# Performance work log

Measured on AMD Instinct MI355X. Metric: run time of the kernel, lower is better.

The kernel has to match this reference:

```python
import jax, jax.numpy as jnp
import numpy as np

# Dims: B nodes, Z species (elements), IN/OUT channels, M = 2*l+1 (l=1)
B, Z, IN, OUT, M = 8192, 10, 512, 512, 3
ALPHA = 1.0 / np.sqrt(IN)  # self.alpha = 1/sqrt(in_dim)
SQRT3 = float(np.sqrt(3.0))


def setup_inputs() -> dict:
    key = jax.random.key(0)
    k1, k2, k3 = jax.random.split(key, 3)
    t = jax.random.normal(k1, (B, IN, M), dtype=jnp.float32)
    species = jax.random.randint(k2, (B,), 0, Z)
    node_attrs = jax.nn.one_hot(species, Z, dtype=jnp.float32)  # [B, Z] one-hot
    # torch.nn.init.uniform_(weights, -sqrt(3), sqrt(3))
    weights = jax.random.uniform(k3, (Z, OUT, IN), dtype=jnp.float32,
                                 minval=-SQRT3, maxval=SQRT3)
    return {"t": t, "node_attrs": node_attrs, "weights": weights}


def reference(t, node_attrs, weights):
    # Faithful to: einsum('bz, zCc, bcd -> bCd', node_attrs, weights*alpha, t)
    # Contract weights with t first per species ([Z,B,C,M], ~500MB), which
    # avoids the huge [B,C,c] per-node weight-gather intermediate, then
    # select/sum over species with the one-hot node_attrs.
    W = weights * ALPHA                       # [Z, OUT, IN]
    zt = jnp.einsum('zCc,bcd->zbCd', W, t)    # [Z, B, OUT, M]
    out = jnp.einsum('bz,zbCd->bCd', node_attrs, zt)  # [B, OUT, M]
    return out
```

## Files before the change

kernel.cpp:

```cpp
#include <hip/hip_runtime.h>
#include <stdint.h>

#define NB   8192
#define NZ   10
#define CIN  512
#define COUT 512
#define MM   3
#define ALPHA 0.04419417382415922f

#define ROWS_TOTAL (NB * MM)
#define BM 256
#define BN 256
#define BK 32
#define NKT (CIN / BK)
#define MAX_MT (ROWS_TOTAL / BM + NZ)
#define NYB (COUT / BN)
#define NWG (MAX_MT * NYB)
#define NGRP 32

typedef short bf16x8 __attribute__((ext_vector_type(8)));
typedef float f32x4  __attribute__((ext_vector_type(4)));

__device__ __forceinline__ uint16_t f2bf(float f) {
    union { float f; uint32_t i; } v; v.f = f;
    uint32_t x = v.i;
    x += 0x7fffu + ((x >> 16) & 1u);
    return (uint16_t)(x >> 16);
}
__device__ __forceinline__ uint32_t pack2(float a, float b) {
    return (uint32_t)f2bf(a) | ((uint32_t)f2bf(b) << 16);
}
__device__ __forceinline__ void async16(const void* g, void* l) {
    __builtin_amdgcn_global_load_lds((const uint32_t*)g, (uint32_t*)l, 16, 0, 0);
}

__global__ __launch_bounds__(256)
void prep_kernel(const float* __restrict__ attrs, const float* __restrict__ w,
                 int* __restrict__ species, int* __restrict__ hist,
                 ushort* __restrict__ wt) {
    const int tid = threadIdx.x;
    if (blockIdx.x >= NGRP) {
        const size_t base = (size_t)(blockIdx.x - NGRP) * 2048;
        const float* src = w + base;
        ushort* dst = wt + base;
        float4 a = *(const float4*)(src + tid * 4);
        float4 b = *(const float4*)(src + 1024 + tid * 4);
        uint2 oa, ob;
        oa.x = pack2(a.x, a.y); oa.y = pack2(a.z, a.w);
        ob.x = pack2(b.x, b.y); ob.y = pack2(b.z, b.w);
        *(uint2*)(dst + tid * 4) = oa;
        *(uint2*)(dst + 1024 + tid * 4) = ob;
        return;
    }
    __shared__ int wc[4][NZ];
    const int b = blockIdx.x * 256 + tid;
    const float* a = attrs + (size_t)b * NZ;
    int s = 0;
    #pragma unroll
    for (int z = 0; z < NZ; z++) if (a[z] > 0.5f) s = z;
    species[b] = s;
    const int wv = tid >> 6, lane = tid & 63;
    #pragma unroll
    for (int z = 0; z < NZ; z++) {
        unsigned long long m = __ballot(s == z);
        if (lane == 0) wc[wv][z] = __popcll(m);
    }
    __syncthreads();
    if (tid < NZ) {
        hist[blockIdx.x * NZ + tid] = wc[0][tid] + wc[1][tid] + wc[2][tid] + wc[3][tid];
    }
}

__global__ __launch_bounds__(256)
void place_kernel(const int* __restrict__ species, const int* __restrict__ hist,
                  int* __restrict__ sorted, int* __restrict__ offsets,
                  int* __restrict__ tile_offsets) {
    __shared__ int lhist[NGRP][NZ];
    __shared__ int loff[NZ + 1], ltoff[NZ + 1];
    __shared__ int pb[NZ];
    __shared__ int wc[4][NZ];
    const int tid = threadIdx.x, g = blockIdx.x;

    for (int i = tid; i < NGRP * NZ; i += 256) ((int*)lhist)[i] = hist[i];
    __syncthreads();
    if (tid == 0) {
        int off = 0, toff = 0;
        for (int z = 0; z < NZ; z++) {
            int tot = 0;
            for (int gg = 0; gg < NGRP; gg++) tot += lhist[gg][z];
            loff[z] = off; ltoff[z] = toff;
            off += tot;
            toff += (3 * tot + BM - 1) / BM;
        }
        loff[NZ] = off; ltoff[NZ] = toff;
    }
    __syncthreads();
    if (tid < NZ) {
        int base = loff[tid];
        for (int gg = 0; gg < g; gg++) base += lhist[gg][tid];
        pb[tid] = base;
    }
    if (g == 0 && tid < NZ + 1) {
        offsets[tid] = loff[tid];
        tile_offsets[tid] = ltoff[tid];
    }
    const int b = g * 256 + tid;
    const int s = species[b];
    const int wv = tid >> 6, lane = tid & 63;
    unsigned long long mymask = 0;
    #pragma unroll
    for (int z = 0; z < NZ; z++) {
        unsigned long long m = __ballot(s == z);
        if (lane == 0) wc[wv][z] = __popcll(m);
        if (s == z) mymask = m;
    }
    __syncthreads();
    int rank = __popcll(mymask & ((1ull << lane) - 1ull));
    #pragma unroll
    for (int w2 = 0; w2 < 4; w2++) if (w2 < wv) rank += wc[w2][s];
    sorted[pb[s] + rank] = b;
}

__global__ __launch_bounds__(256)
void pack_t(const float* __restrict__ t, const int* __restrict__ sorted,
            ushort* __restrict__ tt) {
    const int w = threadIdx.x >> 6, L = threadIdx.x & 63;
    const int p = blockIdx.x * 4 + w;
    const int node = sorted[p];
    const float4* src = (const float4*)(t + (size_t)node * (CIN * MM) + L * 24);
    float4 f[6];
    #pragma unroll
    for (int i = 0; i < 6; i++) f[i] = src[i];
    const float* v = (const float*)f;
    #pragma unroll
    for (int d = 0; d < MM; d++) {
        uint4 o;
        o.x = pack2(v[d],      v[3 + d]);
        o.y = pack2(v[6 + d],  v[9 + d]);
        o.z = pack2(v[12 + d], v[15 + d]);
        o.w = pack2(v[18 + d], v[21 + d]);
        *(uint4*)&tt[(size_t)(3 * p + d) * CIN + L * 8] = o;
    }
}

__global__ __launch_bounds__(512, 2)
void gemm_kernel(const ushort* __restrict__ tt, const ushort* __restrict__ wt,
                 const int* __restrict__ sorted, const int* __restrict__ offsets,
                 const int* __restrict__ tile_offsets, float* __restrict__ out) {
    extern __shared__ __align__(16) ushort smem[];
    __shared__ int spos[96];

    const int bid = blockIdx.x;
    const int xcd = bid & 7, ii = bid >> 3;
    const int wg = (xcd < 4 ? xcd * 27 : 108 + (xcd - 4) * 26) + ii;
    const int tz = wg >> 1;
    const int Cbase = (wg & 1) * BN;

    if (tz >= tile_offsets[NZ]) return;
    int z = 0;
    #pragma unroll
    for (int i = 1; i < NZ; i++) if (tile_offsets[i] <= tz) z = i;

    const int row_base = 3 * offsets[z] + (tz - tile_offsets[z]) * BM;
    const int row_end  = 3 * offsets[z + 1];
    const int pos0     = row_base / 3;

    const int tid = threadIdx.x;
    const int w = tid >> 6, L = tid & 63;
    if (tid < 96) spos[tid] = sorted[min(pos0 + tid, NB - 1)];

    const int lr16 = w * 16 + (L >> 2);
    const int cs   = (L & 3) ^ ((L >> 3) & 3);
    const size_t aoff = (size_t)(row_base + lr16) * CIN + cs * 8;
    const size_t boff = ((size_t)z * COUT + Cbase + lr16) * CIN + cs * 8;

#define ASLOT(s) (smem + (s) * 16384)
#define BSLOT(s) (smem + (s) * 16384 + 8192)
#define STAGE_A(s, kt) do {                                                  \
        async16(tt + aoff + (kt) * BK,                    ASLOT(s) + w * 512);          \
        async16(tt + aoff + (size_t)128 * CIN + (kt) * BK, ASLOT(s) + 4096 + w * 512);  \
    } while (0)
#define STAGE_B(s, kt) do {                                                  \
        async16(wt + boff + (kt) * BK,                    BSLOT(s) + w * 512);          \
        async16(wt + boff + (size_t)128 * CIN + (kt) * BK, BSLOT(s) + 4096 + w * 512);  \
    } while (0)

    const int wm = w & 1, wn = w >> 1;
    const int q = L >> 4, mr = L & 15;
    const int qs = (q ^ ((mr >> 1) & 3)) * 8;

    f32x4 acc[8][4];
    #pragma unroll
    for (int i = 0; i < 8; i++)
        #pragma unroll
        for (int j = 0; j < 4; j++) acc[i][j] = (f32x4){0.f, 0.f, 0.f, 0.f};

    STAGE_A(0, 0); STAGE_B(0, 0);
    STAGE_A(1, 1); STAGE_B(1, 1);

    int cur = 0, stg = 2;
    for (int kt = 0; kt < NKT; kt++) {
        if (kt + 1 < NKT) {
            asm volatile("s_waitcnt vmcnt(4)" ::: "memory");
        } else {
            asm volatile("s_waitcnt vmcnt(0)" ::: "memory");
        }
        asm volatile("s_barrier" ::: "memory");
        if (kt + 2 < NKT) STAGE_A(stg, kt + 2);

        const ushort* Ab = ASLOT(cur);
        const ushort* Bb = BSLOT(cur);
        bf16x8 af[4], bf[4];
        #pragma unroll
        for (int am = 0; am < 4; am++)
            af[am] = *(const bf16x8*)(Ab + (wm * 128 + am * 16 + mr) * 32 + qs);
        #pragma unroll
        for (int bn = 0; bn < 4; bn++)
            bf[bn] = *(const bf16x8*)(Bb + (wn * 64 + bn * 16 + mr) * 32 + qs);
        __builtin_amdgcn_s_setprio(1);
        #pragma unroll
        for (int am = 0; am < 4; am++)
            #pragma unroll
            for (int bn = 0; bn < 4; bn++)
                acc[am][bn] = __builtin_amdgcn_mfma_f32_16x16x32_bf16(
                    af[am], bf[bn], acc[am][bn], 0, 0, 0);
        __builtin_amdgcn_s_setprio(0);

        asm volatile("s_barrier" ::: "memory");
        if (kt + 2 < NKT) STAGE_B(stg, kt + 2);

        bf16x8 ag[4];
        #pragma unroll
        for (int am = 0; am < 4; am++)
            ag[am] = *(const bf16x8*)(Ab + (wm * 128 + (am + 4) * 16 + mr) * 32 + qs);
        __builtin_amdgcn_s_setprio(1);
        #pragma unroll
        for (int am = 0; am < 4; am++)
            #pragma unroll
            for (int bn = 0; bn < 4; bn++)
                acc[am + 4][bn] = __builtin_amdgcn_mfma_f32_16x16x32_bf16(
                    ag[am], bf[bn], acc[am + 4][bn], 0, 0, 0);
        __builtin_amdgcn_s_setprio(0);

        cur = (cur == 2) ? 0 : cur + 1;
        stg = (stg == 2) ? 0 : stg + 1;
    }
#undef STAGE_A
#undef STAGE_B

    float* ebuf = (float*)smem;
    #pragma unroll
    for (int ch = 0; ch < 6; ch++) {
        __syncthreads();
        const int pbase = pos0 + ch * 16;
        #pragma unroll
        for (int am = 0; am < 8; am++) {
            #pragma unroll
            for (int r = 0; r < 4; r++) {
                const int Rg = row_base + wm * 128 + am * 16 + q * 4 + r;
                const int pos = Rg / 3;
                const int d = Rg - 3 * pos;
                const int lp = pos - pbase;
                if (lp >= 0 && lp < 16 && Rg < row_end) {
                    #pragma unroll
                    for (int bn = 0; bn < 4; bn++) {
                        const int c = wn * 64 + bn * 16 + mr;
                        ebuf[(lp * BN + c) * 3 + d] = ALPHA * acc[am][bn][r];
                    }
                }
            }
        }
        __syncthreads();
        #pragma unroll 4
        for (int j = 0; j < 24; j++) {
            const int idx = j * 512 + tid;
            const int lp  = idx / 768;
            const int o   = idx - lp * 768;
            const int pos = pbase + lp;
            const int d   = o % 3;
            const int row = 3 * pos + d;
            if (row >= row_base && row < row_base + BM && row < row_end) {
                const int node = spos[pos - pos0];
                out[(size_t)node * (COUT * MM) + Cbase * 3 + o] = ebuf[idx];
            }
        }
    }
}

extern "C" void kernel_launch(void* const* d_in, const int* in_sizes, int n_in,
                              void* d_out, int out_size, void* d_ws, size_t ws_size,
                              hipStream_t stream) {
    const float* t     = (const float*)d_in[0];
    const float* attrs = (const float*)d_in[1];
    const float* w     = (const float*)d_in[2];
    float* out = (float*)d_out;

    uint8_t* ws = (uint8_t*)d_ws;
    int* species      = (int*)ws;                  ws += NB * 4;
    int* sorted       = (int*)ws;                  ws += NB * 4;
    int* hist         = (int*)ws;                  ws += NGRP * NZ * 4;
    int* offsets      = (int*)ws;                  ws += 16 * 4;
    int* tile_offsets = (int*)ws;                  ws += 16 * 4;
    ws = (uint8_t*)(((uintptr_t)ws + 255) & ~(uintptr_t)255);
    ushort* wt = (ushort*)ws;                      ws += (size_t)NZ * COUT * CIN * 2;
    ushort* tt = (ushort*)ws;

    hipLaunchKernelGGL(prep_kernel, dim3(NGRP + (NZ * COUT * CIN) / 2048), dim3(256),
                       0, stream, attrs, w, species, hist, wt);
    hipLaunchKernelGGL(place_kernel, dim3(NGRP), dim3(256), 0, stream,
                       species, hist, sorted, offsets, tile_offsets);
    hipLaunchKernelGGL(pack_t, dim3(NB / 4), dim3(256), 0, stream, t, sorted, tt);
    hipLaunchKernelGGL(gemm_kernel, dim3(NWG), dim3(512), 3 * 2 * 256 * BK * 2, stream,
                       tt, wt, sorted, offsets, tile_offsets, out);
}
```

Measured before the change: 149.9 us.

## Fuse prep, placement, packing and GEMM into one cooperative grid-synced kernel

```diff
diff --git a/kernel.cpp b/kernel.cpp
--- a/kernel.cpp
+++ b/kernel.cpp
@@ -1,4 +1,5 @@
 #include <hip/hip_runtime.h>
+#include <hip/hip_cooperative_groups.h>
 #include <stdint.h>
 
 #define NB   8192
@@ -17,6 +18,7 @@
 #define NYB (COUT / BN)
 #define NWG (MAX_MT * NYB)
 #define NGRP 32
+#define DYN_LDS (3 * 2 * 256 * BK * 2)
 
 typedef short bf16x8 __attribute__((ext_vector_type(8)));
 typedef float f32x4  __attribute__((ext_vector_type(4)));
@@ -32,6 +34,213 @@
 }
 __device__ __forceinline__ void async16(const void* g, void* l) {
     __builtin_amdgcn_global_load_lds((const uint32_t*)g, (uint32_t*)l, 16, 0, 0);
+}
+
+__global__ __launch_bounds__(512, 2)
+void fused_kernel(const float* __restrict__ t, const float* __restrict__ attrs,
+                  const float* __restrict__ w, float* __restrict__ out,
+                  int* __restrict__ sorted, int* __restrict__ meta,
+                  ushort* __restrict__ wt, ushort* __restrict__ ttn) {
+    extern __shared__ __align__(16) ushort smem[];
+    __shared__ int spos[96];
+    __shared__ int loff[NZ + 1], ltoff[NZ + 1];
+
+    cooperative_groups::grid_group grid = cooperative_groups::this_grid();
+    const int bid = blockIdx.x, tid = threadIdx.x;
+    const int gtid = bid * 512 + tid;
+    const int w8 = tid >> 6, L = tid & 63;
+
+    int mys = 0;
+    if (gtid < NB) {
+        const float* a = attrs + (size_t)gtid * NZ;
+        #pragma unroll
+        for (int z = 0; z < NZ; z++) if (a[z] > 0.5f) mys = z;
+        atomicAdd(&meta[mys], 1);
+    }
+    for (int i = gtid; i < NZ * COUT * CIN / 8; i += NWG * 512) {
+        const float4* src = (const float4*)(w + (size_t)i * 8);
+        float4 a = src[0], b = src[1];
+        uint4 o;
+        o.x = pack2(a.x, a.y); o.y = pack2(a.z, a.w);
+        o.z = pack2(b.x, b.y); o.w = pack2(b.z, b.w);
+        *(uint4*)(wt + (size_t)i * 8) = o;
+    }
+    for (int node = bid * 8 + w8; node < NB; node += NWG * 8) {
+        const float4* src = (const float4*)(t + (size_t)node * (CIN * MM) + L * 24);
+        float4 f[6];
+        #pragma unroll
+        for (int i = 0; i < 6; i++) f[i] = src[i];
+        const float* v = (const float*)f;
+        #pragma unroll
+        for (int d = 0; d < MM; d++) {
+            uint4 o;
+            o.x = pack2(v[d],      v[3 + d]);
+            o.y = pack2(v[6 + d],  v[9 + d]);
+            o.z = pack2(v[12 + d], v[15 + d]);
+            o.w = pack2(v[18 + d], v[21 + d]);
+            *(uint4*)&ttn[(size_t)(3 * node + d) * CIN + L * 8] = o;
+        }
+    }
+
+    grid.sync();
+
+    if (tid == 0) {
+        int off = 0, toff = 0;
+        for (int z = 0; z < NZ; z++) {
+            const int c = atomicAdd(&meta[z], 0);
+            loff[z] = off; ltoff[z] = toff;
+            off += c;
+            toff += (3 * c + BM - 1) / BM;
+        }
+        loff[NZ] = off; ltoff[NZ] = toff;
+    }
+    __syncthreads();
+    if (gtid < NB) {
+        const int p = loff[mys] + atomicAdd(&meta[16 + mys], 1);
+        sorted[p] = gtid;
+    }
+
+    grid.sync();
+
+    const int xcd = bid & 7, ii = bid >> 3;
+    const int wg = (xcd < 4 ? xcd * 27 : 108 + (xcd - 4) * 26) + ii;
+    const int tz = wg >> 1;
+    const int Cbase = (wg & 1) * BN;
+
+    if (tz >= ltoff[NZ]) return;
+    int z = 0;
+    #pragma unroll
+    for (int i = 1; i < NZ; i++) if (ltoff[i] <= tz) z = i;
+
+    const int row_base = 3 * loff[z] + (tz - ltoff[z]) * BM;
+    const int row_end  = 3 * loff[z + 1];
+    const int pos0     = row_base / 3;
+
+    if (tid < 96) spos[tid] = sorted[min(pos0 + tid, NB - 1)];
+
+    const int lr16 = w8 * 16 + (L >> 2);
+    const int cs   = (L & 3) ^ ((L >> 3) & 3);
+    const int R0 = row_base + lr16, R1 = R0 + 128;
+    const int pA0 = R0 / 3, dA0 = R0 - 3 * pA0;
+    const int pA1 = R1 / 3, dA1 = R1 - 3 * pA1;
+    const int nA0 = sorted[min(pA0, NB - 1)];
+    const int nA1 = sorted[min(pA1, NB - 1)];
+    const ushort* gA0 = ttn + (size_t)(3 * nA0 + dA0) * CIN + cs * 8;
+    const ushort* gA1 = ttn + (size_t)(3 * nA1 + dA1) * CIN + cs * 8;
+    const size_t boff = ((size_t)z * COUT + Cbase + lr16) * CIN + cs * 8;
+
+#define ASLOT(s) (smem + (s) * 16384)
+#define BSLOT(s) (smem + (s) * 16384 + 8192)
+#define FSTAGE_A(s, kt) do {                                                  \
+        async16(gA0 + (kt) * BK, ASLOT(s) + w8 * 512);                        \
+        async16(gA1 + (kt) * BK, ASLOT(s) + 4096 + w8 * 512);                 \
+    } while (0)
+#define FSTAGE_B(s, kt) do {                                                  \
+        async16(wt + boff + (kt) * BK, BSLOT(s) + w8 * 512);                  \
+        async16(wt + boff + (size_t)128 * CIN + (kt) * BK,                    \
+                BSLOT(s) + 4096 + w8 * 512);                                  \
+    } while (0)
+
+    const int wm = w8 & 1, wn = w8 >> 1;
+    const int q = L >> 4, mr = L & 15;
+    const int qs = (q ^ ((mr >> 1) & 3)) * 8;
+
+    f32x4 acc[8][4];
+    #pragma unroll
+    for (int i = 0; i < 8; i++)
+        #pragma unroll
+        for (int j = 0; j < 4; j++) acc[i][j] = (f32x4){0.f, 0.f, 0.f, 0.f};
+
+    FSTAGE_A(0, 0); FSTAGE_B(0, 0);
+    FSTAGE_A(1, 1); FSTAGE_B(1, 1);
+
+    int cur = 0, stg = 2;
+    for (int kt = 0; kt < NKT; kt++) {
+        if (kt + 1 < NKT) {
+            asm volatile("s_waitcnt vmcnt(4)" ::: "memory");
+        } else {
+            asm volatile("s_waitcnt vmcnt(0)" ::: "memory");
+        }
+        asm volatile("s_barrier" ::: "memory");
+        if (kt + 2 < NKT) FSTAGE_A(stg, kt + 2);
+
+        const ushort* Ab = ASLOT(cur);
+        const ushort* Bb = BSLOT(cur);
+        bf16x8 af[4], bf[4];
+        #pragma unroll
+        for (int am = 0; am < 4; am++)
+            af[am] = *(const bf16x8*)(Ab + (wm * 128 + am * 16 + mr) * 32 + qs);
+        #pragma unroll
+        for (int bn = 0; bn < 4; bn++)
+            bf[bn] = *(const bf16x8*)(Bb + (wn * 64 + bn * 16 + mr) * 32 + qs);
+        __builtin_amdgcn_s_setprio(1);
+        #pragma unroll
+        for (int am = 0; am < 4; am++)
+            #pragma unroll
+            for (int bn = 0; bn < 4; bn++)
+                acc[am][bn] = __builtin_amdgcn_mfma_f32_16x16x32_bf16(
+                    af[am], bf[bn], acc[am][bn], 0, 0, 0);
+        __builtin_amdgcn_s_setprio(0);
+
+        asm volatile("s_barrier" ::: "memory");
+        if (kt + 2 < NKT) FSTAGE_B(stg, kt + 2);
+
+        bf16x8 ag[4];
+        #pragma unroll
+        for (int am = 0; am < 4; am++)
+            ag[am] = *(const bf16x8*)(Ab + (wm * 128 + (am + 4) * 16 + mr) * 32 + qs);
+        __builtin_amdgcn_s_setprio(1);
+        #pragma unroll
+        for (int am = 0; am < 4; am++)
+            #pragma unroll
+            for (int bn = 0; bn < 4; bn++)
+                acc[am + 4][bn] = __builtin_amdgcn_mfma_f32_16x16x32_bf16(
+                    ag[am], bf[bn], acc[am + 4][bn], 0, 0, 0);
+        __builtin_amdgcn_s_setprio(0);
+
+        cur = (cur == 2) ? 0 : cur + 1;
+        stg = (stg == 2) ? 0 : stg + 1;
+    }
+#undef FSTAGE_A
+#undef FSTAGE_B
+
+    float* ebuf = (float*)smem;
+    #pragma unroll
+    for (int ch = 0; ch < 6; ch++) {
+        __syncthreads();
+        const int pbase = pos0 + ch * 16;
+        #pragma unroll
+        for (int am = 0; am < 8; am++) {
+            #pragma unroll
+            for (int r = 0; r < 4; r++) {
+                const int Rg = row_base + wm * 128 + am * 16 + q * 4 + r;
+                const int pos = Rg / 3;
+                const int d = Rg - 3 * pos;
+                const int lp = pos - pbase;
+                if (lp >= 0 && lp < 16 && Rg < row_end) {
+                    #pragma unroll
+                    for (int bn = 0; bn < 4; bn++) {
+                        const int c = wn * 64 + bn * 16 + mr;
+                        ebuf[(lp * BN + c) * 3 + d] = ALPHA * acc[am][bn][r];
+                    }
+                }
+            }
+        }
+        __syncthreads();
+        #pragma unroll 4
+        for (int j = 0; j < 24; j++) {
+            const int idx = j * 512 + tid;
+            const int lp  = idx / 768;
+            const int o   = idx - lp * 768;
+            const int pos = pbase + lp;
+            const int d   = o % 3;
+            const int row = 3 * pos + d;
+            if (row >= row_base && row < row_base + BM && row < row_end) {
+                const int node = spos[pos - pos0];
+                out[(size_t)node * (COUT * MM) + Cbase * 3 + o] = ebuf[idx];
+            }
+        }
+    }
 }
 
 __global__ __launch_bounds__(256)
@@ -66,9 +275,8 @@
         if (lane == 0) wc[wv][z] = __popcll(m);
     }
     __syncthreads();
-    if (tid < NZ) {
+    if (tid < NZ)
         hist[blockIdx.x * NZ + tid] = wc[0][tid] + wc[1][tid] + wc[2][tid] + wc[3][tid];
-    }
 }
 
 __global__ __launch_bounds__(256)
@@ -174,15 +382,15 @@
     const size_t aoff = (size_t)(row_base + lr16) * CIN + cs * 8;
     const size_t boff = ((size_t)z * COUT + Cbase + lr16) * CIN + cs * 8;
 
-#define ASLOT(s) (smem + (s) * 16384)
-#define BSLOT(s) (smem + (s) * 16384 + 8192)
-#define STAGE_A(s, kt) do {                                                  \
-        async16(tt + aoff + (kt) * BK,                    ASLOT(s) + w * 512);          \
-        async16(tt + aoff + (size_t)128 * CIN + (kt) * BK, ASLOT(s) + 4096 + w * 512);  \
+#define STAGE_A(s, kt) do {                                                   \
+        async16(tt + aoff + (kt) * BK, ASLOT(s) + w * 512);                   \
+        async16(tt + aoff + (size_t)128 * CIN + (kt) * BK,                    \
+                ASLOT(s) + 4096 + w * 512);                                   \
     } while (0)
-#define STAGE_B(s, kt) do {                                                  \
-        async16(wt + boff + (kt) * BK,                    BSLOT(s) + w * 512);          \
-        async16(wt + boff + (size_t)128 * CIN + (kt) * BK, BSLOT(s) + 4096 + w * 512);  \
+#define STAGE_B(s, kt) do {                                                   \
+        async16(wt + boff + (kt) * BK, BSLOT(s) + w * 512);                   \
+        async16(wt + boff + (size_t)128 * CIN + (kt) * BK,                    \
+                BSLOT(s) + 4096 + w * 512);                                   \
     } while (0)
 
     const int wm = w & 1, wn = w >> 1;
@@ -301,15 +509,29 @@
     int* hist         = (int*)ws;                  ws += NGRP * NZ * 4;
     int* offsets      = (int*)ws;                  ws += 16 * 4;
     int* tile_offsets = (int*)ws;                  ws += 16 * 4;
+    int* meta         = (int*)ws;                  ws += 32 * 4;
     ws = (uint8_t*)(((uintptr_t)ws + 255) & ~(uintptr_t)255);
-    ushort* wt = (ushort*)ws;                      ws += (size_t)NZ * COUT * CIN * 2;
-    ushort* tt = (ushort*)ws;
-
-    hipLaunchKernelGGL(prep_kernel, dim3(NGRP + (NZ * COUT * CIN) / 2048), dim3(256),
-                       0, stream, attrs, w, species, hist, wt);
-    hipLaunchKernelGGL(place_kernel, dim3(NGRP), dim3(256), 0, stream,
-                       species, hist, sorted, offsets, tile_offsets);
-    hipLaunchKernelGGL(pack_t, dim3(NB / 4), dim3(256), 0, stream, t, sorted, tt);
-    hipLaunchKernelGGL(gemm_kernel, dim3(NWG), dim3(512), 3 * 2 * 256 * BK * 2, stream,
-                       tt, wt, sorted, offsets, tile_offsets, out);
-}
+    ushort* wt  = (ushort*)ws;                     ws += (size_t)NZ * COUT * CIN * 2;
+    ushort* ttn = (ushort*)ws;
+
+    hipMemsetAsync(meta, 0, 32 * 4, stream);
+
+    hipFuncSetAttribute((const void*)fused_kernel,
+                        hipFuncAttributeMaxDynamicSharedMemorySize, DYN_LDS);
+
+    void* args[] = {(void*)&t, (void*)&attrs, (void*)&w, (void*)&out,
+                    (void*)&sorted, (void*)&meta, (void*)&wt, (void*)&ttn};
+    hipError_t e = hipLaunchCooperativeKernel((const void*)fused_kernel,
+                                              dim3(NWG), dim3(512), args,
+                                              DYN_LDS, stream);
+    if (e != hipSuccess) {
+        hipLaunchKernelGGL(prep_kernel, dim3(NGRP + (NZ * COUT * CIN) / 2048),
+                           dim3(256), 0, stream, attrs, w, species, hist, wt);
+        hipLaunchKernelGGL(place_kernel, dim3(NGRP), dim3(256), 0, stream,
+                           species, hist, sorted, offsets, tile_offsets);
+        hipLaunchKernelGGL(pack_t, dim3(NB / 4), dim3(256), 0, stream,
+                           t, sorted, ttn);
+        hipLaunchKernelGGL(gemm_kernel, dim3(NWG), dim3(512), DYN_LDS, stream,
+                           ttn, wt, sorted, offsets, tile_offsets, out);
+    }
+}
```

New measurement: 248.9 us. 1.66x slower.
